# Optimization experiments

Hardware: AMD Instinct MI355X
Metric: run time of the kernel (lower is better)

## Reference

```python
import jax, jax.numpy as jnp
import numpy as np

H = 28; W = 28; N = H * W
P = N              # padded max persistence pairs per homology dimension
T = 32             # landscape resolution
K1, K2 = 2, 3      # K_max for the two topo layers
M0_1, M0_2 = 0.05, 0.2
LIMS = ((1.0, 28.0), (1.0, 28.0))


def _make_nbrs(h, w, conn8):
    idx = np.arange(h * w).reshape(h, w)
    offs = [(-1, 0), (1, 0), (0, -1), (0, 1)]
    if conn8:
        offs += [(-1, -1), (-1, 1), (1, -1), (1, 1)]
    nbrs = []
    for i in range(h):
        for j in range(w):
            cur = [idx[i + a, j + b] for a, b in offs if 0 <= i + a < h and 0 <= j + b < w]
            nbrs.append(np.asarray(cur, np.int64))
    return nbrs

_NBR4 = _make_nbrs(H, W, False)
_NBR8 = _make_nbrs(H, W, True)


def _h0_pairs(vals, nbrs):
    # 0-dim persistence pairs of a vertex-valued sublevel filtration (union-find, elder rule)
    order = np.argsort(vals, kind="stable")
    pos = np.empty(N, np.int64); pos[order] = np.arange(N)
    parent = np.arange(N); birth = np.arange(N)
    added = np.zeros(N, bool)
    bi = np.zeros(P, np.int32); di = np.zeros(P, np.int32)
    k = 0
    def find(x):
        r = x
        while parent[r] != r: r = parent[r]
        while parent[x] != r: parent[x], x = r, parent[x]
        return r
    for v in order:
        added[v] = True
        for u in nbrs[v]:
            if not added[u]: continue
            ru, rv = find(u), find(v)
            if ru == rv: continue
            if pos[birth[ru]] <= pos[birth[rv]]:
                lb = birth[rv]; parent[rv] = ru
            else:
                lb = birth[ru]; parent[ru] = rv
            if k < P:
                bi[k] = lb; di[k] = v; k += 1
    return bi, di


def _pers_pairs_np(x):
    # x: [M, N] -> (birth_idx, death_idx) each [M, 2, P]; padded pairs point at idx 0 (zero persistence)
    x = np.asarray(x, np.float64)
    M = x.shape[0]
    bi = np.zeros((M, 2, P), np.int32); di = np.zeros((M, 2, P), np.int32)
    for m in range(M):
        b0, d0 = _h0_pairs(x[m], _NBR4)      # H0: sublevel, 4-connectivity
        b1, d1 = _h0_pairs(-x[m], _NBR8)     # H1 by Alexander duality: H0 of superlevel, 8-connectivity
        bi[m, 0], di[m, 0] = b0, d0
        bi[m, 1], di[m, 1] = d1, b1          # H1 birth = vals[d1], death = vals[b1]
    return bi, di


def _grid_d2():
    xs = np.linspace(LIMS[0][0], LIMS[0][1], H)
    ys = np.linspace(LIMS[1][0], LIMS[1][1], W)
    gx, gy = np.meshgrid(xs, ys, indexing="ij")
    pts = np.stack([gx.ravel(), gy.ravel()], 1)              # [N, 2] grid coordinates
    d2 = ((pts[:, None, :] - pts[None, :, :]) ** 2).sum(-1)  # [N, N] squared distances
    si = np.argsort(d2, axis=1, kind="stable")
    return jnp.asarray(si), jnp.asarray(np.take_along_axis(d2, si, 1), jnp.float32)

_SORT_IDX, _D2S = _grid_d2()


def dtm(x_flat, m0):
    # weighted distance-to-measure on the pixel grid, r=2; x_flat: [M, N] positive weights
    bound = m0 * jnp.sum(x_flat, -1, keepdims=True)                        # [M, 1]
    ws = x_flat[:, _SORT_IDX]                                              # [M, N, N] weights in distance order
    cum = jnp.cumsum(ws, -1)
    eff = jnp.minimum(jnp.maximum(bound[..., None] - (cum - ws), 0.0), ws) # effective mass per neighbor
    return jnp.sqrt(jnp.sum(eff * _D2S, -1) / bound)                       # [M, N]


def _landscape(vals, bi, di, start, end, K):
    # persistence landscape lambda_k sampled on T points from (birth, death) critical-vertex indices
    M = vals.shape[0]
    mi = jnp.arange(M)[:, None, None]
    b = vals[mi, bi]; d = vals[mi, di]                                     # [M, 2, P]
    t = jnp.linspace(start, end, T, dtype=vals.dtype)                      # [T]
    tent = jnp.maximum(jnp.minimum(t - b[..., None], d[..., None] - t), 0.0)  # [M, 2, P, T]
    lam, _ = jax.lax.top_k(jnp.swapaxes(tent, -1, -2), K)                  # [M, 2, T, K]
    return jnp.swapaxes(lam, -1, -2).reshape(M, 2 * K * T)                 # [M, dims*K*T]


def pl_features(vals, start, end, K):
    M = vals.shape[0]
    bi, di = jax.pure_callback(
        _pers_pairs_np,
        (jax.ShapeDtypeStruct((M, 2, P), np.int32),
         jax.ShapeDtypeStruct((M, 2, P), np.int32)),
        jax.lax.stop_gradient(vals))
    return _landscape(vals, bi, di, start, end, K)


def setup_inputs():
    key = jax.random.key(0)
    ks = jax.random.split(key, 7)
    B = 64
    return {
        "input": jax.random.uniform(ks[0], (B, 1, H, W), jnp.float32, 1e-3, 1.0),
        "w_g1": 0.1 * jax.random.normal(ks[1], (32, 2 * K1 * T), jnp.float32),
        "b_g1": 0.1 * jax.random.normal(ks[2], (32,), jnp.float32),
        "w_g2": 0.1 * jax.random.normal(ks[3], (32, 2 * K2 * T), jnp.float32),
        "b_g2": 0.1 * jax.random.normal(ks[4], (32,), jnp.float32),
        "w_fc": 0.1 * jax.random.normal(ks[5], (10, 64), jnp.float32),
        "b_fc": 0.1 * jax.random.normal(ks[6], (10,), jnp.float32),
    }


def reference(input, w_g1, b_g1, w_g2, b_g2, w_fc, b_fc):
    x_flat = input.reshape(-1, N)                                        # num_channels = 1
    f1 = dtm(x_flat, M0_1)
    f2 = dtm(x_flat, M0_2)
    x1 = jax.nn.relu(pl_features(f1, 0.0, 7.0, K1) @ w_g1.T + b_g1)      # topo layer 1 (start=0, end=7, K=2)
    x2 = jax.nn.relu(pl_features(f2, 1.0, 8.0, K2) @ w_g2.T + b_g2)      # topo layer 2 (start=1, end=8, K=3)
    return jnp.concatenate([x1, x2], -1) @ w_fc.T + b_fc                 # [B, num_classes]
```

## Files before the change

kernel.cpp:

```cpp
#include <hip/hip_runtime.h>

#define HW 28
#define NPIX 784
#define NIMG 64
#define MAXREC 5504
#define NOFF 3025
#define NOFFP 3072
#define ND2 1459

#define DXPK 41048u
#define DYPK 34949u

struct alignas(16) OffTbl { unsigned int t[NOFFP]; };

static constexpr OffTbl make_offtbl() {
    OffTbl o{};
    int cnt[ND2] = {};
    for (int dx = -27; dx <= 27; ++dx)
        for (int dy = -27; dy <= 27; ++dy)
            cnt[dx * dx + dy * dy]++;
    int pos[ND2] = {};
    int run = 0;
    for (int b = 0; b < ND2; ++b) { pos[b] = run; run += cnt[b]; }
    int lin_[NOFF] = {}, dxs[NOFF] = {}, dys[NOFF] = {};
    int p2[ND2] = {};
    for (int b = 0; b < ND2; ++b) p2[b] = pos[b];
    for (int dx = -27; dx <= 27; ++dx)
        for (int dy = -27; dy <= 27; ++dy) {
            int d2 = dx * dx + dy * dy;
            int s = p2[d2]++;
            lin_[s] = dx * HW + dy; dxs[s] = dx; dys[s] = dy;
        }
    for (int b = 0; b < ND2; ++b) {
        int s0 = pos[b], s1 = pos[b] + cnt[b];
        for (int a = s0 + 1; a < s1; ++a) {
            int L = lin_[a], X = dxs[a], Y = dys[a];
            int c = a;
            while (c > s0 && lin_[c - 1] > L) {
                lin_[c] = lin_[c - 1]; dxs[c] = dxs[c - 1]; dys[c] = dys[c - 1];
                --c;
            }
            lin_[c] = L; dxs[c] = X; dys[c] = Y;
        }
    }
    for (int s = 0; s < NOFF; ++s)
        o.t[s] = ((unsigned)(dxs[s] * dxs[s] + dys[s] * dys[s]) << 16) |
                 ((unsigned)(dxs[s] + 27) << 8) | (unsigned)(dys[s] + 27);
    for (int s = NOFF; s < NOFFP; ++s) o.t[s] = 0xFFFFFFFFu;
    return o;
}

__device__ const OffTbl OTBC = make_offtbl();

__global__ void xt_sums_kernel(const float* __restrict__ x,
                               float* __restrict__ sums,
                               float* __restrict__ xT) {
    int tid = threadIdx.x;
    int m = blockIdx.x;
    const float* xr = x + m * NPIX;
    float acc = 0.f;
    for (int j = tid; j < NPIX; j += 256) {
        float v = xr[j];
        xT[j * NIMG + m] = v;
        acc += v;
    }
    for (int off = 32; off > 0; off >>= 1) acc += __shfl_down(acc, off, 64);
    __shared__ float red[4];
    int lane = tid & 63, w = tid >> 6;
    if (lane == 0) red[w] = acc;
    __syncthreads();
    if (tid == 0) sums[m] = red[0] + red[1] + red[2] + red[3];
}

__global__ void __launch_bounds__(256) sortdtm_kernel(const float* __restrict__ xT,
                                                      const float* __restrict__ sums,
                                                      float* __restrict__ F) {
    __shared__ unsigned int tpl[NPIX];
    __shared__ int wtot[4];
    int tid = threadIdx.x;
    int i = blockIdx.x;
    int ii = i / HW, ij = i % HW;

    const uint4* o4 = (const uint4*)OTBC.t + tid * 3;
    uint4 qa = o4[0], qb = o4[1], qc = o4[2];
    unsigned int ent[12] = {qa.x, qa.y, qa.z, qa.w,
                            qb.x, qb.y, qb.z, qb.w,
                            qc.x, qc.y, qc.z, qc.w};
    int ct = 0;
    #pragma unroll
    for (int e = 0; e < 12; ++e) {
        int dx = (int)((ent[e] >> 8) & 255u) - 27;
        int dy = (int)(ent[e] & 255u) - 27;
        ct += ((unsigned)(ii + dx) < (unsigned)HW && (unsigned)(ij + dy) < (unsigned)HW) ? 1 : 0;
    }
    int lane = tid & 63, wv = tid >> 6;
    int p = ct;
    for (int off = 1; off < 64; off <<= 1) {
        int t2 = __shfl_up(p, off, 64);
        if (lane >= off) p += t2;
    }
    if (lane == 63) wtot[wv] = p;
    __syncthreads();
    int slot = p - ct;
    for (int w2 = 0; w2 < wv; ++w2) slot += wtot[w2];
    #pragma unroll
    for (int e = 0; e < 12; ++e) {
        int dx = (int)((ent[e] >> 8) & 255u) - 27;
        int dy = (int)(ent[e] & 255u) - 27;
        int ui = ii + dx, uj = ij + dy;
        if ((unsigned)ui < (unsigned)HW && (unsigned)uj < (unsigned)HW) {
            tpl[slot] = (unsigned)(ui * HW + uj) | (ent[e] & 0xFFFF0000u);
            ++slot;
        }
    }
    __syncthreads();

    if (tid < 64) {
        float s = sums[tid];
        float bound1 = 0.05f * s, bound2 = 0.2f * s;
        float cum = 0.f, acc1 = 0.f, acc2 = 0.f;
        for (int t0 = 0; t0 < NPIX; t0 += 16) {
            unsigned int e[16];
            #pragma unroll
            for (int u = 0; u < 16; ++u) e[u] = tpl[t0 + u];
            float w[16];
            #pragma unroll
            for (int u = 0; u < 16; ++u) w[u] = xT[(e[u] & 0xffffu) * NIMG + tid];
            #pragma unroll
            for (int u = 0; u < 16; ++u) {
                float d2 = (float)(e[u] >> 16);
                float ce = cum;
                cum += w[u];
                acc1 += fminf(fmaxf(bound1 - ce, 0.f), w[u]) * d2;
                acc2 += fminf(fmaxf(bound2 - ce, 0.f), w[u]) * d2;
            }
            if (__ballot(cum < bound2) == 0ull) break;
        }
        F[0 * NIMG * NPIX + tid * NPIX + i] = sqrtf(acc1 / bound1);
        F[1 * NIMG * NPIX + tid * NPIX + i] = sqrtf(acc2 / bound2);
    }
}

template<int NN>
__device__ int uf_basin_run(const int* posA, const int* ordA,
                            int* bas, unsigned int* pb, int* comp,
                            int* recs, int* pairsI,
                            int2* mergeLDS, int* shInts, int* wtot16) {
    const int tid = threadIdx.x;
    const int lane = tid & 63, wv = tid >> 6;

    for (int s = tid; s < NPIX; s += 1024) {
        int si = s / HW, sj = s % HW;
        int bestPos = posA[s], best = s;
        #pragma unroll
        for (int o = 0; o < NN; ++o) {
            int dx = ((DXPK >> (2 * o)) & 3) - 1;
            int dy = ((DYPK >> (2 * o)) & 3) - 1;
            int ui = si + dx, uj = sj + dy;
            if ((unsigned)ui < (unsigned)HW && (unsigned)uj < (unsigned)HW) {
                int u = ui * HW + uj;
                int pu = posA[u];
                if (pu < bestPos) { bestPos = pu; best = u; }
            }
        }
        bas[s] = best;
    }
    __syncthreads();

    for (int it = 0; it < 10; ++it) {
        int changed = 0;
        for (int s = tid; s < NPIX; s += 1024) {
            int b = bas[s];
            int bb = bas[b];
            if (bb != b) { bas[s] = bb; changed = 1; }
        }
        if (__syncthreads_count(changed) == 0) break;
    }

    for (int s = tid; s < NPIX; s += 1024)
        pb[s] = ((unsigned)posA[s] << 10) | (unsigned)bas[s];
    __syncthreads();

    int nrec = 0;
    {
        int r = tid;
        int cnt = 0;
        int myr[NN - 1];
        int got[NN - 1];
        #pragma unroll
        for (int t = 0; t < NN - 1; ++t) { got[t] = -1; myr[t] = 0; }
        if (r > 0 && r < NPIX) {
            int v = ordA[r];
            int vi = v / HW, vj = v % HW;
            int pivot = (int)(pb[v] & 1023u);
            #pragma unroll
            for (int o = 0; o < NN; ++o) {
                int dx = ((DXPK >> (2 * o)) & 3) - 1;
                int dy = ((DYPK >> (2 * o)) & 3) - 1;
                int ui = vi + dx, uj = vj + dy;
                if ((unsigned)ui < (unsigned)HW && (unsigned)uj < (unsigned)HW) {
                    int u = ui * HW + uj;
                    unsigned e = pb[u];
                    if ((int)(e >> 10) < r) {
                        int b = (int)(e & 1023u);
                        bool dup = (b == pivot);
                        #pragma unroll
                        for (int t = 0; t < NN - 1; ++t) dup = dup || (got[t] == b);
                        if (!dup) {
                            #pragma unroll
                            for (int t = 0; t < NN - 1; ++t)
                                if (t == cnt) { got[t] = b; myr[t] = (v << 20) | (pivot << 10) | b; }
                            cnt++;
                        }
                    }
                }
            }
        }
        int p = cnt;
        for (int off = 1; off < 64; off <<= 1) {
            int t2 = __shfl_up(p, off, 64);
            if (lane >= off) p += t2;
        }
        if (lane == 63) wtot16[wv] = p;
        __syncthreads();
        int wadd = 0;
        for (int w2 = 0; w2 < wv; ++w2) wadd += wtot16[w2];
        int tot = 0;
        #pragma unroll
        for (int w2 = 0; w2 < 16; ++w2) tot += wtot16[w2];
        int excl = wadd + p - cnt;
        #pragma unroll
        for (int t = 0; t < NN - 1; ++t)
            if (t < cnt) recs[excl + t] = myr[t];
        nrec = tot;
        __syncthreads();
    }

    int k = 0;
    for (int base = 0; base < nrec; base += 64) {
        int nrem = 0;
        if (wv == 0) {
            int idx = base + lane;
            int rec = (idx < nrec) ? recs[idx] : 0;
            int pa = (rec >> 10) & 1023, pbn = rec & 1023;
            int ka = 0, kb = 0;
            if (idx < nrec) { ka = comp[pa]; kb = comp[pbn]; }
            for (;;) {
                unsigned long long d = __ballot(ka != kb);
                if (d == 0ull) break;
                int i = (int)__ffsll((long long)d) - 1;
                int sA = __builtin_amdgcn_readlane(ka, i);
                int sB = __builtin_amdgcn_readlane(kb, i);
                int w = min(sA, sB), l = max(sA, sB);
                int sv = __builtin_amdgcn_readlane(rec, i) >> 20;
                if (lane == 0) {
                    pairsI[k] = (l & 1023) | (sv << 10);
                    mergeLDS[nrem] = make_int2(l, w);
                }
                k++;
                ka = (ka == l) ? w : ka;
                kb = (kb == l) ? w : kb;
                nrem++;
                if (nrem == 63) {
                    for (int s = lane; s < NPIX; s += 64) {
                        int cv = comp[s], c0 = cv;
                        for (int e = 0; e < nrem; ++e) {
                            int2 me = mergeLDS[e];
                            cv = (cv == me.x) ? me.y : cv;
                        }
                        if (cv != c0) comp[s] = cv;
                    }
                    if (idx < nrec) { ka = comp[pa]; kb = comp[pbn]; }
                    nrem = 0;
                }
            }
            if (lane == 0) shInts[0] = nrem;
        }
        __syncthreads();
        int nr = shInts[0];
        if (nr > 0) {
            for (int s = tid; s < NPIX; s += 1024) {
                int cv = comp[s], c0 = cv;
                for (int e = 0; e < nr; ++e) {
                    int2 me = mergeLDS[e];
                    cv = (cv == me.x) ? me.y : cv;
                }
                if (cv != c0) comp[s] = cv;
            }
        }
        __syncthreads();
    }
    if (tid == 0) shInts[1] = k;
    __syncthreads();
    return shInts[1];
}

__global__ void __launch_bounds__(1024) uf_land_kernel(const float* __restrict__ F,
                                                       float* __restrict__ LAM1,
                                                       float* __restrict__ LAM2) {
    __shared__ int posA[NPIX], ordA[NPIX], bas[NPIX], comp[NPIX], pairsI[NPIX];
    __shared__ unsigned int pbArr[NPIX];
    __shared__ alignas(16) unsigned long long key64[NPIX];
    __shared__ float fv[NPIX];
    __shared__ int recs[MAXREC];
    __shared__ int2 mergeLDS[64];
    __shared__ int shInts[2];
    __shared__ int wtot16[16];
    int tid = threadIdx.x;
    int task = blockIdx.x;
    int feat = task >> 7;
    int dir = (task >> 6) & 1;
    int m = task & 63;
    const float* fr = F + feat * NIMG * NPIX + m * NPIX;

    for (int j = tid; j < NPIX; j += 1024) {
        float f = fr[j];
        fv[j] = f;
        unsigned int b = __float_as_uint(f);
        if (dir) b = ~b;
        key64[j] = ((unsigned long long)b << 10) | (unsigned)j;
    }
    __syncthreads();

    if (tid < NPIX) {
        unsigned long long pki = key64[tid];
        int rank = 0;
        const ulonglong2* k2 = (const ulonglong2*)key64;
        for (int c = 0; c < NPIX / 2; ++c) {
            ulonglong2 kv = k2[c];
            rank += (int)(kv.x < pki) + (int)(kv.y < pki);
        }
        posA[tid] = rank;
        ordA[rank] = tid;
    }
    __syncthreads();
    for (int s = tid; s < NPIX; s += 1024) comp[s] = (posA[s] << 10) | s;

    int k;
    if (dir == 0) k = uf_basin_run<4>(posA, ordA, bas, pbArr, comp, recs, pairsI,
                                      mergeLDS, shInts, wtot16);
    else          k = uf_basin_run<8>(posA, ordA, bas, pbArr, comp, recs, pairsI,
                                      mergeLDS, shInts, wtot16);

    if (tid < 32) {
        int t = tid;
        float start = (feat == 0) ? 0.f : 1.f;
        float end   = (feat == 0) ? 7.f : 8.f;
        float tv = start + (end - start) * ((float)t / 31.f);
        float v0 = 0.f, v1 = 0.f, v2 = 0.f;
        for (int p = 0; p < k; ++p) {
            int pi = pairsI[p];
            float fb = fv[pi & 1023], fd = fv[pi >> 10];
            float bb = dir ? fd : fb;
            float dd = dir ? fb : fd;
            float tent = fmaxf(fminf(tv - bb, dd - tv), 0.f);
            if (tent > v0)      { v2 = v1; v1 = v0; v0 = tent; }
            else if (tent > v1) { v2 = v1; v1 = tent; }
            else if (tent > v2) { v2 = tent; }
        }
        if (feat == 0) {
            float* lam = LAM1 + m * 128 + dir * 64;
            lam[0 * 32 + t] = v0;
            lam[1 * 32 + t] = v1;
        } else {
            float* lam = LAM2 + m * 192 + dir * 96;
            lam[0 * 32 + t] = v0;
            lam[1 * 32 + t] = v1;
            lam[2 * 32 + t] = v2;
        }
    }
}

__global__ void mlp_kernel(const float* __restrict__ LAM1, const float* __restrict__ LAM2,
                           const float* __restrict__ w1, const float* __restrict__ b1,
                           const float* __restrict__ w2, const float* __restrict__ b2,
                           const float* __restrict__ wf, const float* __restrict__ bf,
                           float* __restrict__ out) {
    __shared__ float xc[64];
    int m = blockIdx.x;
    int n = threadIdx.x;
    if (n < 32) {
        float acc = b1[n];
        const float* l = LAM1 + m * 128;
        for (int c = 0; c < 128; ++c) acc += w1[n * 128 + c] * l[c];
        xc[n] = fmaxf(acc, 0.f);
    } else {
        int n2 = n - 32;
        float acc = b2[n2];
        const float* l = LAM2 + m * 192;
        for (int c = 0; c < 192; ++c) acc += w2[n2 * 192 + c] * l[c];
        xc[n] = fmaxf(acc, 0.f);
    }
    __syncthreads();
    if (n < 10) {
        float acc = bf[n];
        for (int c = 0; c < 64; ++c) acc += wf[n * 64 + c] * xc[c];
        out[m * 10 + n] = acc;
    }
}

extern "C" void kernel_launch(void* const* d_in, const int* in_sizes, int n_in,
                              void* d_out, int out_size, void* d_ws, size_t ws_size,
                              hipStream_t stream) {
    const float* x  = (const float*)d_in[0];
    const float* w1 = (const float*)d_in[1];
    const float* b1 = (const float*)d_in[2];
    const float* w2 = (const float*)d_in[3];
    const float* b2 = (const float*)d_in[4];
    const float* wf = (const float*)d_in[5];
    const float* bf = (const float*)d_in[6];
    float* out = (float*)d_out;

    char* ws = (char*)d_ws;
    size_t off = 0;
    float* XT   = (float*)(ws + off); off += (size_t)NPIX * NIMG * 4;
    float* SUMS = (float*)(ws + off); off += 256;
    float* F    = (float*)(ws + off); off += (size_t)2 * NIMG * NPIX * 4;
    float* LAM1 = (float*)(ws + off); off += (size_t)NIMG * 128 * 4;
    float* LAM2 = (float*)(ws + off); off += (size_t)NIMG * 192 * 4;

    xt_sums_kernel<<<NIMG, 256, 0, stream>>>(x, SUMS, XT);
    sortdtm_kernel<<<NPIX, 256, 0, stream>>>(XT, SUMS, F);
    uf_land_kernel<<<256, 1024, 0, stream>>>(F, LAM1, LAM2);
    mlp_kernel<<<NIMG, 64, 0, stream>>>(LAM1, LAM2, w1, b1, w2, b2, wf, bf, out);
}
```

Before: 118.7 us.

## Process four merge records per lane and parallelize landscape top-k across block

The single-wave merge loop now handles 256 records per batch, four per lane, loaded as int4 and folded into one ballot per iteration. This cuts the number of outer batches and block-wide barriers. The landscape tent top-3 computation now spreads over all 1024 threads in 32 strided subsets, then a 32-thread pass reduces the partial top-3 lists kept in the reused recs buffer. MAXREC grows so the int4 reads stay in bounds, which adds a per-lane select chain and slightly more LDS.

After: 123.8 us. 1.04x slower.

```diff
diff --git a/kernel.cpp b/kernel.cpp
--- a/kernel.cpp
+++ b/kernel.cpp
@@ -3,7 +3,7 @@
 #define HW 28
 #define NPIX 784
 #define NIMG 64
-#define MAXREC 5504
+#define MAXREC 5632
 #define NOFF 3025
 #define NOFFP 3072
 #define ND2 1459
@@ -237,29 +237,47 @@
     }
 
     int k = 0;
-    for (int base = 0; base < nrec; base += 64) {
+    for (int base = 0; base < nrec; base += 256) {
         int nrem = 0;
         if (wv == 0) {
-            int idx = base + lane;
-            int rec = (idx < nrec) ? recs[idx] : 0;
-            int pa = (rec >> 10) & 1023, pbn = rec & 1023;
-            int ka = 0, kb = 0;
-            if (idx < nrec) { ka = comp[pa]; kb = comp[pbn]; }
+            int idx0 = base + lane * 4;
+            int4 rl = *(const int4*)&recs[idx0];
+            int rec4[4] = {rl.x, rl.y, rl.z, rl.w};
+            int ka[4], kb[4];
+            #pragma unroll
+            for (int q = 0; q < 4; ++q) {
+                if (idx0 + q >= nrec) rec4[q] = 0;
+                int pa = (rec4[q] >> 10) & 1023, pbn = rec4[q] & 1023;
+                ka[q] = comp[pa]; kb[q] = comp[pbn];
+            }
             for (;;) {
-                unsigned long long d = __ballot(ka != kb);
+                int selKa = ka[3], selKb = kb[3], selRec = rec4[3];
+                bool has = (ka[3] != kb[3]);
+                #pragma unroll
+                for (int q = 2; q >= 0; --q) {
+                    bool u = (ka[q] != kb[q]);
+                    selKa  = u ? ka[q]  : selKa;
+                    selKb  = u ? kb[q]  : selKb;
+                    selRec = u ? rec4[q] : selRec;
+                    has = has || u;
+                }
+                unsigned long long d = __ballot(has);
                 if (d == 0ull) break;
                 int i = (int)__ffsll((long long)d) - 1;
-                int sA = __builtin_amdgcn_readlane(ka, i);
-                int sB = __builtin_amdgcn_readlane(kb, i);
+                int sA = __builtin_amdgcn_readlane(selKa, i);
+                int sB = __builtin_amdgcn_readlane(selKb, i);
                 int w = min(sA, sB), l = max(sA, sB);
-                int sv = __builtin_amdgcn_readlane(rec, i) >> 20;
+                int sv = __builtin_amdgcn_readlane(selRec, i) >> 20;
                 if (lane == 0) {
                     pairsI[k] = (l & 1023) | (sv << 10);
                     mergeLDS[nrem] = make_int2(l, w);
                 }
                 k++;
-                ka = (ka == l) ? w : ka;
-                kb = (kb == l) ? w : kb;
+                #pragma unroll
+                for (int q = 0; q < 4; ++q) {
+                    ka[q] = (ka[q] == l) ? w : ka[q];
+                    kb[q] = (kb[q] == l) ? w : kb[q];
+                }
                 nrem++;
                 if (nrem == 63) {
                     for (int s = lane; s < NPIX; s += 64) {
@@ -270,7 +288,11 @@
                         }
                         if (cv != c0) comp[s] = cv;
                     }
-                    if (idx < nrec) { ka = comp[pa]; kb = comp[pbn]; }
+                    #pragma unroll
+                    for (int q = 0; q < 4; ++q) {
+                        int pa = (rec4[q] >> 10) & 1023, pbn = rec4[q] & 1023;
+                        ka[q] = comp[pa]; kb[q] = comp[pbn];
+                    }
                     nrem = 0;
                 }
             }
@@ -302,7 +324,7 @@
     __shared__ unsigned int pbArr[NPIX];
     __shared__ alignas(16) unsigned long long key64[NPIX];
     __shared__ float fv[NPIX];
-    __shared__ int recs[MAXREC];
+    __shared__ alignas(16) int recs[MAXREC];
     __shared__ int2 mergeLDS[64];
     __shared__ int shInts[2];
     __shared__ int wtot16[16];
@@ -342,13 +364,14 @@
     else          k = uf_basin_run<8>(posA, ordA, bas, pbArr, comp, recs, pairsI,
                                       mergeLDS, shInts, wtot16);
 
-    if (tid < 32) {
-        int t = tid;
-        float start = (feat == 0) ? 0.f : 1.f;
-        float end   = (feat == 0) ? 7.f : 8.f;
+    float start = (feat == 0) ? 0.f : 1.f;
+    float end   = (feat == 0) ? 7.f : 8.f;
+    {
+        int sub = tid >> 5;
+        int t = tid & 31;
         float tv = start + (end - start) * ((float)t / 31.f);
         float v0 = 0.f, v1 = 0.f, v2 = 0.f;
-        for (int p = 0; p < k; ++p) {
+        for (int p = sub; p < k; p += 32) {
             int pi = pairsI[p];
             float fb = fv[pi & 1023], fd = fv[pi >> 10];
             float bb = dir ? fd : fb;
@@ -357,6 +380,25 @@
             if (tent > v0)      { v2 = v1; v1 = v0; v0 = tent; }
             else if (tent > v1) { v2 = v1; v1 = tent; }
             else if (tent > v2) { v2 = tent; }
+        }
+        float* part = (float*)recs;
+        int bse = (sub * 32 + t) * 3;
+        part[bse] = v0; part[bse + 1] = v1; part[bse + 2] = v2;
+    }
+    __syncthreads();
+    if (tid < 32) {
+        int t = tid;
+        const float* part = (const float*)recs;
+        float v0 = 0.f, v1 = 0.f, v2 = 0.f;
+        for (int s2 = 0; s2 < 32; ++s2) {
+            int bse = (s2 * 32 + t) * 3;
+            #pragma unroll
+            for (int q = 0; q < 3; ++q) {
+                float x = part[bse + q];
+                if (x > v0)      { v2 = v1; v1 = v0; v0 = x; }
+                else if (x > v1) { v2 = v1; v1 = x; }
+                else if (x > v2) { v2 = x; }
+            }
         }
         if (feat == 0) {
             float* lam = LAM1 + m * 128 + dir * 64;
```

## Replace batched component relabeling with single-wave merge-log replay

Applied to the files above, without the earlier changes.

The union-find merge phase now runs entirely in wavefront 0. It keeps a growing log of all merges in LDS and replays that log on each chunk's component labels instead of periodically rewriting the whole comp array. This removes the block-wide barriers and 784-pixel relabel passes per 64-record chunk. The trade-off is that each chunk's replay cost grows with the number of merges already made, and the merge log array is enlarged.

New measurement: 120.7 us. Within noise of the previous version (+1.7%).

```diff
diff --git a/kernel.cpp b/kernel.cpp
--- a/kernel.cpp
+++ b/kernel.cpp
@@ -237,14 +237,17 @@
     }
 
     int k = 0;
-    for (int base = 0; base < nrec; base += 64) {
-        int nrem = 0;
-        if (wv == 0) {
+    if (wv == 0) {
+        for (int base = 0; base < nrec; base += 64) {
             int idx = base + lane;
             int rec = (idx < nrec) ? recs[idx] : 0;
             int pa = (rec >> 10) & 1023, pbn = rec & 1023;
-            int ka = 0, kb = 0;
-            if (idx < nrec) { ka = comp[pa]; kb = comp[pbn]; }
+            int ka = comp[pa], kb = comp[pbn];
+            for (int e = 0; e < k; ++e) {
+                int2 me = mergeLDS[e];
+                ka = (ka == me.x) ? me.y : ka;
+                kb = (kb == me.x) ? me.y : kb;
+            }
             for (;;) {
                 unsigned long long d = __ballot(ka != kb);
                 if (d == 0ull) break;
@@ -255,42 +258,15 @@
                 int sv = __builtin_amdgcn_readlane(rec, i) >> 20;
                 if (lane == 0) {
                     pairsI[k] = (l & 1023) | (sv << 10);
-                    mergeLDS[nrem] = make_int2(l, w);
+                    mergeLDS[k] = make_int2(l, w);
                 }
                 k++;
                 ka = (ka == l) ? w : ka;
                 kb = (kb == l) ? w : kb;
-                nrem++;
-                if (nrem == 63) {
-                    for (int s = lane; s < NPIX; s += 64) {
-                        int cv = comp[s], c0 = cv;
-                        for (int e = 0; e < nrem; ++e) {
-                            int2 me = mergeLDS[e];
-                            cv = (cv == me.x) ? me.y : cv;
-                        }
-                        if (cv != c0) comp[s] = cv;
-                    }
-                    if (idx < nrec) { ka = comp[pa]; kb = comp[pbn]; }
-                    nrem = 0;
-                }
-            }
-            if (lane == 0) shInts[0] = nrem;
-        }
-        __syncthreads();
-        int nr = shInts[0];
-        if (nr > 0) {
-            for (int s = tid; s < NPIX; s += 1024) {
-                int cv = comp[s], c0 = cv;
-                for (int e = 0; e < nr; ++e) {
-                    int2 me = mergeLDS[e];
-                    cv = (cv == me.x) ? me.y : cv;
-                }
-                if (cv != c0) comp[s] = cv;
-            }
-        }
-        __syncthreads();
-    }
-    if (tid == 0) shInts[1] = k;
+            }
+        }
+        if (lane == 0) shInts[1] = k;
+    }
     __syncthreads();
     return shInts[1];
 }
@@ -303,7 +279,7 @@
     __shared__ alignas(16) unsigned long long key64[NPIX];
     __shared__ float fv[NPIX];
     __shared__ int recs[MAXREC];
-    __shared__ int2 mergeLDS[64];
+    __shared__ int2 mergeLDS[NPIX];
     __shared__ int shInts[2];
     __shared__ int wtot16[16];
     int tid = threadIdx.x;
```
